# Kernel optimization log

Hardware: AMD Instinct MI355X
Metric: run time of the kernel (lower is better)

Reference implementation:

```python
import jax, jax.numpy as jnp
import numpy as np

N = 100000  # num nodes
E = 3200000  # num edges (before self-loops)


def setup_inputs() -> dict:
    key = jax.random.key(0)
    k1, k2, k3, k4 = jax.random.split(key, 4)
    x = jax.random.normal(k1, (N, 128), dtype=jnp.float32)
    edge_index = jax.random.randint(k2, (2, E), 0, N, dtype=jnp.int64)
    W1 = jax.random.normal(k3, (128, 64), dtype=jnp.float32) * (1.0 / np.sqrt(128))
    b1 = jnp.zeros((64,), dtype=jnp.float32)
    W2 = jax.random.normal(k4, (64, 1), dtype=jnp.float32) * (1.0 / np.sqrt(64))
    b2 = jnp.zeros((1,), dtype=jnp.float32)
    return {"x": x, "edge_index": edge_index, "W1": W1, "b1": b1, "W2": W2, "b2": b2}


def _gcn_norm(edge_index, num_nodes):
    # add self-loops, then symmetric normalization deg^-1/2[row]*deg^-1/2[col]
    loops = jnp.arange(num_nodes, dtype=edge_index.dtype)
    row = jnp.concatenate([edge_index[0], loops])  # destination
    col = jnp.concatenate([edge_index[1], loops])  # source
    deg = jax.ops.segment_sum(jnp.ones_like(row, dtype=jnp.float32), row,
                              num_segments=num_nodes)
    dinv = jnp.where(deg > 0, jax.lax.rsqrt(deg), 0.0)
    norm = dinv[row] * dinv[col]  # [E+N]
    return row, col, norm


def _gcn_conv(x, row, col, norm, W, b, num_nodes):
    h = x @ W                                   # transform before propagate
    msg = h[col] * norm[:, None]                # gather + scale  [E+N, out]
    out = jax.ops.segment_sum(msg, row, num_segments=num_nodes)  # scatter-add
    return out + b


def reference(x, edge_index, W1, b1, W2, b2):
    row, col, norm = _gcn_norm(edge_index, N)
    h = _gcn_conv(x, row, col, norm, W1, b1, N)
    h = jax.nn.relu(h)
    # dropout p=0.0 -> identity
    h = _gcn_conv(h, row, col, norm, W2, b2, N)
    return jax.nn.sigmoid(h)
```

## Files before the change

kernel.cpp:

```cpp
#include <hip/hip_runtime.h>
#include <hip/hip_bf16.h>
#include <math.h>

#define BKT_SHIFT 8
#define BKT_W     256
#define NBP       512
#define CHUNK     8192
#define CAPR      9216
#define CAPC      10240

__global__ void init_k(const unsigned* __restrict__ e, int* __restrict__ flag,
                       int* __restrict__ bcur, int nb) {
  int t = blockIdx.x * blockDim.x + threadIdx.x;
  if (t == 0) {
    int z = (e[1] == 0u) + (e[3] == 0u) + (e[5] == 0u) + (e[7] == 0u);
    *flag = (z == 4) ? 1 : 0;
  }
  if (t < nb) bcur[t] = t * CAPR;
}

__global__ __launch_bounds__(512) void bin_k(const void* __restrict__ ei, int* __restrict__ bcur,
                                             unsigned* __restrict__ recs, const int* __restrict__ flag,
                                             int E, int NB) {
  __shared__ unsigned srec[CHUNK];
  __shared__ int h[NBP], scex[NBP], cur[NBP], gb[NBP], s[NBP];
  int t = threadIdx.x;
  h[t] = 0;
  __syncthreads();
  bool f64 = (*flag) != 0;
  int start = blockIdx.x * CHUNK;
  int cntE = min(CHUNK, E - start);
  int r[16], c[16];
#pragma unroll
  for (int j = 0; j < 16; ++j) {
    int i = t + j * 512;
    int e = start + min(i, cntE - 1);
    if (f64) {
      r[j] = (int)((const long long*)ei)[e];
      c[j] = (int)((const long long*)ei)[(long long)E + e];
    } else {
      r[j] = ((const int*)ei)[e];
      c[j] = ((const int*)ei)[E + e];
    }
    if (i < cntE) atomicAdd(&h[r[j] >> BKT_SHIFT], 1);
  }
  __syncthreads();
  int v = h[t];
  s[t] = v;
  __syncthreads();
  for (int d = 1; d < NBP; d <<= 1) {
    int a = (t >= d) ? s[t - d] : 0;
    __syncthreads();
    s[t] += a;
    __syncthreads();
  }
  scex[t] = s[t] - v;
  cur[t] = s[t] - v;
  __syncthreads();
  if (t < NB && v) gb[t] = atomicAdd(&bcur[t], v);
#pragma unroll
  for (int j = 0; j < 16; ++j) {
    int i = t + j * 512;
    if (i < cntE) {
      int b = r[j] >> BKT_SHIFT;
      int slot = atomicAdd(&cur[b], 1);
      srec[slot] = ((unsigned)(r[j] & (BKT_W - 1)) << 17) | (unsigned)c[j];
    }
  }
  __syncthreads();
  for (int i = t; i < cntE; i += 512) {
    int lo = 0, hi = NB - 1;
    while (lo < hi) { int mid = (lo + hi + 1) >> 1; if (scex[mid] <= i) lo = mid; else hi = mid - 1; }
    recs[gb[lo] + (i - scex[lo])] = srec[i];
  }
}

__global__ __launch_bounds__(256) void csr_k(const unsigned* __restrict__ recs,
                                             const int* __restrict__ bcur,
                                             int* __restrict__ csr, int* __restrict__ offs,
                                             int* __restrict__ degs, float* __restrict__ dinv, int N) {
  __shared__ unsigned colbuf[CAPC];
  __shared__ int cnt[BKT_W], scx[BKT_W], cur[BKT_W], tmp[BKT_W];
  __shared__ int wtot;
  int t = threadIdx.x;
  int b = blockIdx.x;
  int rbase = b * CAPR;
  int size = min(bcur[b] - rbase, CAPR);
  int cbase = b * CAPC;
  int nb0 = b << BKT_SHIFT;
  int nNodes = min(BKT_W, N - nb0);
  cnt[t] = 0;
  __syncthreads();
  for (int i = t; i < size; i += 256) atomicAdd(&cnt[recs[rbase + i] >> 17], 1);
  __syncthreads();
  int seg = (cnt[t] + 3) & ~3;
  tmp[t] = seg;
  __syncthreads();
  for (int d = 1; d < BKT_W; d <<= 1) {
    int a = (t >= d) ? tmp[t - d] : 0;
    __syncthreads();
    tmp[t] += a;
    __syncthreads();
  }
  scx[t] = tmp[t] - seg;
  cur[t] = tmp[t] - seg;
  if (t == BKT_W - 1) wtot = tmp[t];
  __syncthreads();
  for (int i = t; i < size; i += 256) {
    unsigned rec = recs[rbase + i];
    int lr = rec >> 17;
    int slot = atomicAdd(&cur[lr], 1);
    colbuf[slot] = rec & 0x1FFFFu;
  }
  __syncthreads();
  int wt = wtot;
  for (int i = t; i < wt; i += 256) csr[cbase + i] = colbuf[i];
  if (t < nNodes) {
    offs[nb0 + t] = cbase + scx[t];
    degs[nb0 + t] = cnt[t];
    dinv[nb0 + t] = rsqrtf((float)(cnt[t] + 1));
  }
}

__device__ __forceinline__ float rlf(float v, int l) {
  return __int_as_float(__builtin_amdgcn_readlane(__float_as_int(v), l));
}

__global__ __launch_bounds__(256) void gemm_k(const float* __restrict__ x,
                                              const float* __restrict__ W1,
                                              const float* __restrict__ dinv,
                                              __hip_bfloat16* __restrict__ q, int n) {
  int lane = threadIdx.x & 63;
  int wave = blockIdx.x * 4 + (threadIdx.x >> 6);
  int nw = gridDim.x * 4;
  float w[128];
#pragma unroll
  for (int k = 0; k < 128; ++k) w[k] = W1[k * 64 + lane];
  int npair = n >> 1;
  const float4* x4 = (const float4*)x;
  for (int p = wave; p < npair; p += nw) {
    float4 xv = x4[p * 64 + lane];
    float a0 = 0.f, b0 = 0.f, c0 = 0.f, d0 = 0.f;
    float a1 = 0.f, b1 = 0.f, c1 = 0.f, d1 = 0.f;
#pragma unroll
    for (int j = 0; j < 32; ++j) {
      a0 = fmaf(rlf(xv.x, j), w[4 * j + 0], a0);
      b0 = fmaf(rlf(xv.y, j), w[4 * j + 1], b0);
      c0 = fmaf(rlf(xv.z, j), w[4 * j + 2], c0);
      d0 = fmaf(rlf(xv.w, j), w[4 * j + 3], d0);
    }
#pragma unroll
    for (int j = 32; j < 64; ++j) {
      int k4 = j - 32;
      a1 = fmaf(rlf(xv.x, j), w[4 * k4 + 0], a1);
      b1 = fmaf(rlf(xv.y, j), w[4 * k4 + 1], b1);
      c1 = fmaf(rlf(xv.z, j), w[4 * k4 + 2], c1);
      d1 = fmaf(rlf(xv.w, j), w[4 * k4 + 3], d1);
    }
    int r0 = 2 * p;
    q[(size_t)r0 * 64 + lane]       = __float2bfloat16(dinv[r0] * ((a0 + b0) + (c0 + d0)));
    q[(size_t)(r0 + 1) * 64 + lane] = __float2bfloat16(dinv[r0 + 1] * ((a1 + b1) + (c1 + d1)));
  }
}

__device__ __forceinline__ float bflo(unsigned u) { return __uint_as_float(u << 16); }
__device__ __forceinline__ float bfhi(unsigned u) { return __uint_as_float(u & 0xFFFF0000u); }

__global__ __launch_bounds__(256) void agg1_k(const __hip_bfloat16* __restrict__ q,
                                              const int* __restrict__ offs,
                                              const int* __restrict__ degs,
                                              const int* __restrict__ csr,
                                              const float* __restrict__ dinv,
                                              const float* __restrict__ b1,
                                              const float* __restrict__ W2,
                                              float* __restrict__ p, int n) {
  int lane = threadIdx.x & 63;
  int node = blockIdx.x * 4 + (threadIdx.x >> 6);
  if (node >= n) return;
  int grp = lane >> 3;
  int fl = lane & 7;
  int o0 = offs[node];
  int deg = degs[node];
  const uint4* qrows = (const uint4*)q;
  float acc[8] = {0.f, 0.f, 0.f, 0.f, 0.f, 0.f, 0.f, 0.f};
  for (int base = 0; base < deg; base += 32) {
    int e4 = base + grp * 4;
    int4 idx = *(const int4*)(csr + o0 + e4);
    int cc0 = (e4 + 0 < deg) ? idx.x : 0;
    int cc1 = (e4 + 1 < deg) ? idx.y : 0;
    int cc2 = (e4 + 2 < deg) ? idx.z : 0;
    int cc3 = (e4 + 3 < deg) ? idx.w : 0;
    float w0 = (e4 + 0 < deg) ? 1.f : 0.f;
    float w1 = (e4 + 1 < deg) ? 1.f : 0.f;
    float w2 = (e4 + 2 < deg) ? 1.f : 0.f;
    float w3 = (e4 + 3 < deg) ? 1.f : 0.f;
    uint4 v0 = qrows[(size_t)cc0 * 8 + fl];
    uint4 v1 = qrows[(size_t)cc1 * 8 + fl];
    uint4 v2 = qrows[(size_t)cc2 * 8 + fl];
    uint4 v3 = qrows[(size_t)cc3 * 8 + fl];
    acc[0] = fmaf(w0, bflo(v0.x), acc[0]); acc[1] = fmaf(w0, bfhi(v0.x), acc[1]);
    acc[2] = fmaf(w0, bflo(v0.y), acc[2]); acc[3] = fmaf(w0, bfhi(v0.y), acc[3]);
    acc[4] = fmaf(w0, bflo(v0.z), acc[4]); acc[5] = fmaf(w0, bfhi(v0.z), acc[5]);
    acc[6] = fmaf(w0, bflo(v0.w), acc[6]); acc[7] = fmaf(w0, bfhi(v0.w), acc[7]);
    acc[0] = fmaf(w1, bflo(v1.x), acc[0]); acc[1] = fmaf(w1, bfhi(v1.x), acc[1]);
    acc[2] = fmaf(w1, bflo(v1.y), acc[2]); acc[3] = fmaf(w1, bfhi(v1.y), acc[3]);
    acc[4] = fmaf(w1, bflo(v1.z), acc[4]); acc[5] = fmaf(w1, bfhi(v1.z), acc[5]);
    acc[6] = fmaf(w1, bflo(v1.w), acc[6]); acc[7] = fmaf(w1, bfhi(v1.w), acc[7]);
    acc[0] = fmaf(w2, bflo(v2.x), acc[0]); acc[1] = fmaf(w2, bfhi(v2.x), acc[1]);
    acc[2] = fmaf(w2, bflo(v2.y), acc[2]); acc[3] = fmaf(w2, bfhi(v2.y), acc[3]);
    acc[4] = fmaf(w2, bflo(v2.z), acc[4]); acc[5] = fmaf(w2, bfhi(v2.z), acc[5]);
    acc[6] = fmaf(w2, bflo(v2.w), acc[6]); acc[7] = fmaf(w2, bfhi(v2.w), acc[7]);
    acc[0] = fmaf(w3, bflo(v3.x), acc[0]); acc[1] = fmaf(w3, bfhi(v3.x), acc[1]);
    acc[2] = fmaf(w3, bflo(v3.y), acc[2]); acc[3] = fmaf(w3, bfhi(v3.y), acc[3]);
    acc[4] = fmaf(w3, bflo(v3.z), acc[4]); acc[5] = fmaf(w3, bfhi(v3.z), acc[5]);
    acc[6] = fmaf(w3, bflo(v3.w), acc[6]); acc[7] = fmaf(w3, bfhi(v3.w), acc[7]);
  }
#pragma unroll
  for (int j = 0; j < 8; ++j) {
    acc[j] += __shfl_xor(acc[j], 8);
    acc[j] += __shfl_xor(acc[j], 16);
    acc[j] += __shfl_xor(acc[j], 32);
  }
  uint4 vs = qrows[(size_t)node * 8 + fl];
  float qs[8] = {bflo(vs.x), bfhi(vs.x), bflo(vs.y), bfhi(vs.y),
                 bflo(vs.z), bfhi(vs.z), bflo(vs.w), bfhi(vs.w)};
  float di = dinv[node];
  float4 bb0 = ((const float4*)b1)[fl * 2], bb1 = ((const float4*)b1)[fl * 2 + 1];
  float4 ww0 = ((const float4*)W2)[fl * 2], ww1 = ((const float4*)W2)[fl * 2 + 1];
  float bbv[8] = {bb0.x, bb0.y, bb0.z, bb0.w, bb1.x, bb1.y, bb1.z, bb1.w};
  float w2v[8] = {ww0.x, ww0.y, ww0.z, ww0.w, ww1.x, ww1.y, ww1.z, ww1.w};
  float tacc = 0.f;
#pragma unroll
  for (int j = 0; j < 8; ++j)
    tacc += fmaxf(fmaf(di, acc[j] + qs[j], bbv[j]), 0.f) * w2v[j];
  tacc += __shfl_xor(tacc, 1); tacc += __shfl_xor(tacc, 2); tacc += __shfl_xor(tacc, 4);
  if (lane == 0) p[node] = di * tacc;
}

__global__ __launch_bounds__(256) void agg2_k(const float* __restrict__ p,
                                              const int* __restrict__ offs,
                                              const int* __restrict__ degs,
                                              const int* __restrict__ csr,
                                              const float* __restrict__ dinv,
                                              const float* __restrict__ b2,
                                              float* __restrict__ out, int n) {
  int lane = threadIdx.x & 63;
  int node = blockIdx.x * 4 + (threadIdx.x >> 6);
  if (node >= n) return;
  int o0 = offs[node];
  int dg = degs[node];
  float s = 0.f;
  for (int e = lane; e < dg; e += 64) s += p[csr[o0 + e]];
  s += __shfl_xor(s, 1); s += __shfl_xor(s, 2); s += __shfl_xor(s, 4);
  s += __shfl_xor(s, 8); s += __shfl_xor(s, 16); s += __shfl_xor(s, 32);
  if (lane == 0) {
    float z = fmaf(dinv[node], s + p[node], b2[0]);
    out[node] = 1.f / (1.f + expf(-z));
  }
}

extern "C" void kernel_launch(void* const* d_in, const int* in_sizes, int n_in,
                              void* d_out, int out_size, void* d_ws, size_t ws_size,
                              hipStream_t stream) {
  const float* x  = (const float*)d_in[0];
  const void*  ei = d_in[1];
  const float* W1 = (const float*)d_in[2];
  const float* b1 = (const float*)d_in[3];
  const float* W2 = (const float*)d_in[4];
  const float* b2 = (const float*)d_in[5];
  float* out = (float*)d_out;
  const int N = in_sizes[0] / 128;
  const int E = in_sizes[1] / 2;
  const int NB = (N + BKT_W - 1) >> BKT_SHIFT;
  const int nchunks = (E + CHUNK - 1) / CHUNK;
  (void)n_in; (void)out_size; (void)ws_size;

  char* base = (char*)d_ws;
  size_t off = 0;
  auto alloc = [&](size_t bytes) -> void* {
    void* ptr = base + off;
    off += (bytes + 1023) & ~(size_t)1023;
    return ptr;
  };
  int*   flag = (int*)alloc(64);
  int*   bcur = (int*)alloc((size_t)NBP * 4);
  int*   offs = (int*)alloc((size_t)N * 4);
  int*   degs = (int*)alloc((size_t)N * 4);
  float* dinv = (float*)alloc((size_t)N * 4);
  unsigned* recs = (unsigned*)alloc((size_t)NB * CAPR * 4);
  int*   csr  = (int*)alloc((size_t)NB * CAPC * 4);
  __hip_bfloat16* q = (__hip_bfloat16*)alloc((size_t)N * 64 * 2);
  float* p    = (float*)alloc((size_t)N * 4);

  init_k<<<1, 512, 0, stream>>>((const unsigned*)ei, flag, bcur, NBP);
  bin_k<<<nchunks, 512, 0, stream>>>(ei, bcur, recs, flag, E, NB);
  csr_k<<<NB, 256, 0, stream>>>(recs, bcur, csr, offs, degs, dinv, N);
  gemm_k<<<512, 256, 0, stream>>>(x, W1, dinv, q, N);
  agg1_k<<<(N + 3) / 4, 256, 0, stream>>>(q, offs, degs, csr, dinv, b1, W2, p, N);
  agg2_k<<<(N + 3) / 4, 256, 0, stream>>>(p, offs, degs, csr, dinv, b2, out, N);
}
```

Baseline: 195.1 us.

## Rewrite dense transform as LDS-tiled GEMM with 4x4 register blocking

After: 168.2 us. 13.8% less time.

```diff
diff --git a/kernel.cpp b/kernel.cpp
--- a/kernel.cpp
+++ b/kernel.cpp
@@ -122,44 +122,87 @@
   }
 }
 
-__device__ __forceinline__ float rlf(float v, int l) {
-  return __int_as_float(__builtin_amdgcn_readlane(__float_as_int(v), l));
+__device__ __forceinline__ unsigned short f2bs(float v) {
+  __hip_bfloat16 b = __float2bfloat16(v);
+  return *reinterpret_cast<unsigned short*>(&b);
 }
 
 __global__ __launch_bounds__(256) void gemm_k(const float* __restrict__ x,
                                               const float* __restrict__ W1,
                                               const float* __restrict__ dinv,
                                               __hip_bfloat16* __restrict__ q, int n) {
-  int lane = threadIdx.x & 63;
-  int wave = blockIdx.x * 4 + (threadIdx.x >> 6);
-  int nw = gridDim.x * 4;
-  float w[128];
-#pragma unroll
-  for (int k = 0; k < 128; ++k) w[k] = W1[k * 64 + lane];
-  int npair = n >> 1;
-  const float4* x4 = (const float4*)x;
-  for (int p = wave; p < npair; p += nw) {
-    float4 xv = x4[p * 64 + lane];
-    float a0 = 0.f, b0 = 0.f, c0 = 0.f, d0 = 0.f;
-    float a1 = 0.f, b1 = 0.f, c1 = 0.f, d1 = 0.f;
-#pragma unroll
-    for (int j = 0; j < 32; ++j) {
-      a0 = fmaf(rlf(xv.x, j), w[4 * j + 0], a0);
-      b0 = fmaf(rlf(xv.y, j), w[4 * j + 1], b0);
-      c0 = fmaf(rlf(xv.z, j), w[4 * j + 2], c0);
-      d0 = fmaf(rlf(xv.w, j), w[4 * j + 3], d0);
-    }
-#pragma unroll
-    for (int j = 32; j < 64; ++j) {
-      int k4 = j - 32;
-      a1 = fmaf(rlf(xv.x, j), w[4 * k4 + 0], a1);
-      b1 = fmaf(rlf(xv.y, j), w[4 * k4 + 1], b1);
-      c1 = fmaf(rlf(xv.z, j), w[4 * k4 + 2], c1);
-      d1 = fmaf(rlf(xv.w, j), w[4 * k4 + 3], d1);
-    }
-    int r0 = 2 * p;
-    q[(size_t)r0 * 64 + lane]       = __float2bfloat16(dinv[r0] * ((a0 + b0) + (c0 + d0)));
-    q[(size_t)(r0 + 1) * 64 + lane] = __float2bfloat16(dinv[r0 + 1] * ((a1 + b1) + (c1 + d1)));
+  __shared__ float4 xs[64 * 32];
+  __shared__ float4 ws[64 * 16];
+  int t = threadIdx.x;
+  int row0 = blockIdx.x * 64;
+  const float4* xg = (const float4*)x;
+  const float4* wg = (const float4*)W1;
+#pragma unroll
+  for (int i = 0; i < 8; ++i) {
+    int flat = t + i * 256;
+    int r = flat >> 5, c = flat & 31;
+    int gr = min(row0 + r, n - 1);
+    xs[r * 32 + (c ^ (r & 31))] = xg[(size_t)gr * 32 + c];
+  }
+  int c4g = t & 15;
+  int r4g = t >> 4;
+  float acc[4][4];
+#pragma unroll
+  for (int j = 0; j < 4; ++j)
+#pragma unroll
+    for (int cc = 0; cc < 4; ++cc) acc[j][cc] = 0.f;
+#pragma unroll
+  for (int h = 0; h < 2; ++h) {
+    if (h) __syncthreads();
+#pragma unroll
+    for (int i = 0; i < 4; ++i) {
+      int flat = t + i * 256;
+      ws[flat] = wg[(h * 64 + (flat >> 4)) * 16 + (flat & 15)];
+    }
+    __syncthreads();
+#pragma unroll 2
+    for (int k4 = 0; k4 < 16; ++k4) {
+      float4 xv[4], wv[4];
+#pragma unroll
+      for (int j = 0; j < 4; ++j) {
+        int r = r4g * 4 + j;
+        xv[j] = xs[r * 32 + ((h * 16 + k4) ^ (r & 31))];
+      }
+#pragma unroll
+      for (int kk = 0; kk < 4; ++kk) wv[kk] = ws[(k4 * 4 + kk) * 16 + c4g];
+#pragma unroll
+      for (int j = 0; j < 4; ++j) {
+        acc[j][0] = fmaf(xv[j].x, wv[0].x, acc[j][0]);
+        acc[j][1] = fmaf(xv[j].x, wv[0].y, acc[j][1]);
+        acc[j][2] = fmaf(xv[j].x, wv[0].z, acc[j][2]);
+        acc[j][3] = fmaf(xv[j].x, wv[0].w, acc[j][3]);
+        acc[j][0] = fmaf(xv[j].y, wv[1].x, acc[j][0]);
+        acc[j][1] = fmaf(xv[j].y, wv[1].y, acc[j][1]);
+        acc[j][2] = fmaf(xv[j].y, wv[1].z, acc[j][2]);
+        acc[j][3] = fmaf(xv[j].y, wv[1].w, acc[j][3]);
+        acc[j][0] = fmaf(xv[j].z, wv[2].x, acc[j][0]);
+        acc[j][1] = fmaf(xv[j].z, wv[2].y, acc[j][1]);
+        acc[j][2] = fmaf(xv[j].z, wv[2].z, acc[j][2]);
+        acc[j][3] = fmaf(xv[j].z, wv[2].w, acc[j][3]);
+        acc[j][0] = fmaf(xv[j].w, wv[3].x, acc[j][0]);
+        acc[j][1] = fmaf(xv[j].w, wv[3].y, acc[j][1]);
+        acc[j][2] = fmaf(xv[j].w, wv[3].z, acc[j][2]);
+        acc[j][3] = fmaf(xv[j].w, wv[3].w, acc[j][3]);
+      }
+    }
+  }
+#pragma unroll
+  for (int j = 0; j < 4; ++j) {
+    int r = row0 + r4g * 4 + j;
+    if (r < n) {
+      float di = dinv[r];
+      ushort4 o;
+      o.x = f2bs(di * acc[j][0]);
+      o.y = f2bs(di * acc[j][1]);
+      o.z = f2bs(di * acc[j][2]);
+      o.w = f2bs(di * acc[j][3]);
+      ((uint2*)q)[(size_t)r * 16 + c4g] = *reinterpret_cast<uint2*>(&o);
+    }
   }
 }
 
@@ -295,7 +338,7 @@
   init_k<<<1, 512, 0, stream>>>((const unsigned*)ei, flag, bcur, NBP);
   bin_k<<<nchunks, 512, 0, stream>>>(ei, bcur, recs, flag, E, NB);
   csr_k<<<NB, 256, 0, stream>>>(recs, bcur, csr, offs, degs, dinv, N);
-  gemm_k<<<512, 256, 0, stream>>>(x, W1, dinv, q, N);
+  gemm_k<<<(N + 63) / 64, 256, 0, stream>>>(x, W1, dinv, q, N);
   agg1_k<<<(N + 3) / 4, 256, 0, stream>>>(q, offs, degs, csr, dinv, b1, W2, p, N);
   agg2_k<<<(N + 3) / 4, 256, 0, stream>>>(p, offs, degs, csr, dinv, b2, out, N);
 }
```
